# Performance work log

Measured on AMD Instinct MI355X. Metric: run time of the kernel, lower is better.

## Reference

```python
import jax, jax.numpy as jnp
import numpy as np

N_HEAD = 16
D_MODEL = 1024
B, C = 4, 2048

def setup_inputs() -> dict:
    key = jax.random.key(0)
    k_x, k_wq, k_bq, k_wo, k_bo = jax.random.split(key, 5)
    s = 0.02
    return {
        "x": jax.random.normal(k_x, (B, C, D_MODEL), dtype=jnp.float32),
        "W_qkv": jax.random.normal(k_wq, (D_MODEL, 3 * D_MODEL), dtype=jnp.float32) * s,
        "b_qkv": jax.random.normal(k_bq, (3 * D_MODEL,), dtype=jnp.float32) * s,
        "W_o": jax.random.normal(k_wo, (D_MODEL, D_MODEL), dtype=jnp.float32) * s,
        "b_o": jax.random.normal(k_bo, (D_MODEL,), dtype=jnp.float32) * s,
    }

def reference(x, W_qkv, b_qkv, W_o, b_o):
    Bsz, Cq, D = x.shape
    H = N_HEAD
    hd = D // H
    qkv = x @ W_qkv + b_qkv                      # [B,C,3D]
    Q, K, V = jnp.split(qkv, 3, axis=2)
    # [B,C,H,hd] -> [B,H,C,hd]
    Q = Q.reshape(Bsz, Cq, H, hd).transpose(0, 2, 1, 3)
    K = K.reshape(Bsz, Cq, H, hd).transpose(0, 2, 1, 3)
    V = V.reshape(Bsz, Cq, H, hd).transpose(0, 2, 1, 3)
    scale = 1.0 / np.sqrt(hd).astype(np.float32)
    att = jnp.einsum('bhqd,bhkd->bhqk', Q, K) * scale
    causal = jnp.tril(jnp.ones((Cq, Cq), dtype=bool))
    att = jnp.where(causal, att, jnp.float32(-jnp.inf))
    att = jax.nn.softmax(att, axis=-1)           # dropout = identity (eval)
    out = jnp.einsum('bhqk,bhkd->bhqd', att, V)  # [B,H,C,hd]
    out = out.transpose(0, 2, 1, 3).reshape(Bsz, Cq, D)
    return out @ W_o + b_o
```

## Files before the change

### kernel.cpp

```cpp
#include <hip/hip_runtime.h>
#include <hip/hip_bf16.h>

typedef __attribute__((ext_vector_type(8))) short bf16x8;
typedef __attribute__((ext_vector_type(4))) float f32x4;

#define NH 16
#define DM 1024
#define HD 64
#define CSEQ 2048
#define MROWS 8192
#define NBH 64

static __device__ __forceinline__ unsigned short f2bf(float f) {
  __hip_bfloat16 h = __float2bfloat16(f);
  return *reinterpret_cast<unsigned short*>(&h);
}

static __device__ __forceinline__ short bf_qscale(short s) {
  unsigned u = ((unsigned)(unsigned short)s) << 16;
  float f = __builtin_bit_cast(float, u) * 0.18033688f;
  return (short)f2bf(f);
}

static __device__ __forceinline__ void gload_lds16(const void* g, void* l) {
  __builtin_amdgcn_global_load_lds(
      (const __attribute__((address_space(1))) unsigned int*)g,
      (__attribute__((address_space(3))) unsigned int*)l, 16, 0, 0);
}

__global__ __launch_bounds__(256) void cast_f32_bf16(const float* __restrict__ in,
                                                     unsigned short* __restrict__ out,
                                                     int n4) {
  int stride = gridDim.x * blockDim.x;
  for (int i = blockIdx.x * blockDim.x + threadIdx.x; i < n4; i += stride) {
    float4 v = ((const float4*)in)[i];
    ushort4 o;
    o.x = f2bf(v.x); o.y = f2bf(v.y); o.z = f2bf(v.z); o.w = f2bf(v.w);
    ((ushort4*)out)[i] = o;
  }
}

__global__ __launch_bounds__(256) void transpose_cast(const float* __restrict__ src,
                                                      unsigned short* __restrict__ dst,
                                                      int K, int N) {
  __shared__ float tile[32][33];
  int tx = threadIdx.x, ty = threadIdx.y;
  int n0 = blockIdx.x * 32, k0 = blockIdx.y * 32;
  #pragma unroll
  for (int i = 0; i < 32; i += 8)
    tile[ty + i][tx] = src[(size_t)(k0 + ty + i) * N + n0 + tx];
  __syncthreads();
  #pragma unroll
  for (int i = 0; i < 32; i += 8)
    dst[(size_t)(n0 + ty + i) * K + k0 + tx] = f2bf(tile[tx][ty + i]);
}

template<int CNT>
static __device__ __forceinline__ void ld_frags(const char* base, int r0, int cx, int g,
                                                bf16x8 (*out)[2]) {
  #pragma unroll
  for (int i = 0; i < CNT; i++) {
    int row = r0 + i * 16 + cx;
    #pragma unroll
    for (int kc = 0; kc < 2; kc++)
      out[i][kc] = *(const bf16x8*)(base + row * 128 + ((((kc << 2) | g) ^ (row & 7)) << 4));
  }
}

#define BARR() __builtin_amdgcn_s_barrier()
#define LGKM0() asm volatile("s_waitcnt lgkmcnt(0)" ::: "memory")
#define VMCNT8() asm volatile("s_waitcnt vmcnt(8)" ::: "memory")
#define VMCNT0() asm volatile("s_waitcnt vmcnt(0)" ::: "memory")
#define PRIO1() __builtin_amdgcn_s_setprio(1)
#define PRIO0() __builtin_amdgcn_s_setprio(0)

static __device__ __forceinline__ void mfma_pair(const bf16x8 af[4][2], const bf16x8 bf2[2][2],
                                                 f32x4 acc[4][4], int n0) {
  #pragma unroll
  for (int kc = 0; kc < 2; kc++)
    #pragma unroll
    for (int mi = 0; mi < 4; mi++)
      #pragma unroll
      for (int ni = 0; ni < 2; ni++)
        acc[mi][n0 + ni] = __builtin_amdgcn_mfma_f32_16x16x32_bf16(
            af[mi][kc], bf2[ni][kc], acc[mi][n0 + ni], 0, 0, 0);
}

template<int MODE>
__global__ __launch_bounds__(256, 2) void gemm128d(const unsigned short* __restrict__ A,
                                                   const unsigned short* __restrict__ BT,
                                                   const float* __restrict__ bias,
                                                   float* __restrict__ outF,
                                                   unsigned short* __restrict__ outQKV,
                                                   int N, int K) {
  __shared__ char sA[2][16384];
  __shared__ char sB[2][16384];
  int tid = threadIdx.x;
  int w = tid >> 6, l = tid & 63, g = l >> 4, cx = l & 15;
  int wm = (w >> 1) * 64, wn = (w & 1) * 64;

  int nwgx = gridDim.x;
  int nwg = nwgx * gridDim.y;
  int gid = blockIdx.y * nwgx + blockIdx.x;
  int swz = (gid & 7) * (nwg >> 3) + (gid >> 3);
  int bm = (swz / nwgx) * 128, bn = (swz % nwgx) * 128;

  const unsigned short* Ap[4];
  const unsigned short* Bp[4];
  #pragma unroll
  for (int i = 0; i < 4; i++) {
    int c = tid + i * 256;
    int ar = c >> 3, as = ((c & 7) ^ (ar & 7)) * 8;
    Ap[i] = A + (size_t)(bm + ar) * K + as;
    Bp[i] = BT + (size_t)(bn + ar) * K + as;
  }

  #define STAGE_AB(t, buf) do { int ko_ = (t) << 6;                 \
      gload_lds16(Ap[0] + ko_, sA[buf] + (tid)       * 16);         \
      gload_lds16(Ap[1] + ko_, sA[buf] + (tid + 256) * 16);         \
      gload_lds16(Ap[2] + ko_, sA[buf] + (tid + 512) * 16);         \
      gload_lds16(Ap[3] + ko_, sA[buf] + (tid + 768) * 16);         \
      gload_lds16(Bp[0] + ko_, sB[buf] + (tid)       * 16);         \
      gload_lds16(Bp[1] + ko_, sB[buf] + (tid + 256) * 16);         \
      gload_lds16(Bp[2] + ko_, sB[buf] + (tid + 512) * 16);         \
      gload_lds16(Bp[3] + ko_, sB[buf] + (tid + 768) * 16);         \
    } while (0)

  f32x4 acc[4][4];
  #pragma unroll
  for (int i = 0; i < 4; i++)
    #pragma unroll
    for (int j = 0; j < 4; j++) acc[i][j] = (f32x4){0.f, 0.f, 0.f, 0.f};

  int NT = K >> 6;

  STAGE_AB(0, 0);
  STAGE_AB(1, 1);
  VMCNT8();
  BARR();

  int cur = 0;
  for (int t = 0; t < NT; t++) {
    const char* Ac = sA[cur];
    const char* Bc = sB[cur];
    bool h1 = (t + 1) < NT, h2 = (t + 2) < NT;
    bf16x8 af[4][2], bfr[4][2];

    ld_frags<4>(Ac, wm, cx, g, af);
    ld_frags<4>(Bc, wn, cx, g, bfr);
    BARR(); LGKM0();
    PRIO1(); mfma_pair(af, &bfr[0], acc, 0); PRIO0();
    BARR();

    if (h2) STAGE_AB(t + 2, cur);
    PRIO1(); mfma_pair(af, &bfr[2], acc, 2); PRIO0();
    if (h2)      { VMCNT8(); }
    else if (h1) { VMCNT0(); }
    BARR();
    cur ^= 1;
  }

  #pragma unroll
  for (int mi = 0; mi < 4; mi++) {
    #pragma unroll
    for (int ni = 0; ni < 4; ni++) {
      int col = bn + wn + ni * 16 + cx;
      float bv = bias[col];
      int row0 = bm + wm + mi * 16 + g * 4;
      #pragma unroll
      for (int r = 0; r < 4; r++) {
        float v = acc[mi][ni][r] + bv;
        int rr = row0 + r;
        if (MODE == 0) {
          outF[(size_t)rr * N + col] = v;
        } else {
          int which = col >> 10, rem = col & 1023;
          int h = rem >> 6, d = rem & 63;
          int b = rr >> 11, cq = rr & 2047;
          if (which == 2) {
            int pos = (cq & ~31) + (((cq >> 2) & 3) << 3) + (((cq >> 4) & 1) << 2) + (cq & 3);
            outQKV[((size_t)2 * NBH + b * NH + h) * (CSEQ * HD) +
                   (size_t)d * CSEQ + pos] = f2bf(v);
          } else {
            outQKV[((size_t)which * NBH + b * NH + h) * (CSEQ * HD) + (size_t)cq * HD + d] = f2bf(v);
          }
        }
      }
    }
  }
  #undef STAGE_AB
}

__global__ __launch_bounds__(256, 2) void attn_kernel(const unsigned short* __restrict__ Qb,
                                                      const unsigned short* __restrict__ Kb,
                                                      const unsigned short* __restrict__ VTb,
                                                      unsigned short* __restrict__ O) {
  __shared__ char sKb[2][16384];
  __shared__ char sVt[2][16384];
  int tid = threadIdx.x;
  int w = tid >> 6, l = tid & 63, g = l >> 4, cx = l & 15;
  int gid = blockIdx.x;
  int bh = ((gid >> 7) << 3) | (gid & 7);
  int qt = 15 - ((gid >> 3) & 15);

  const unsigned short* Qp  = Qb  + (size_t)bh * CSEQ * HD;
  const unsigned short* Kp  = Kb  + (size_t)bh * CSEQ * HD;
  const unsigned short* VTp = VTb + (size_t)bh * CSEQ * HD;

  bf16x8 qf[2][2];
  #pragma unroll
  for (int qh = 0; qh < 2; qh++) {
    int qrow = qt * 128 + w * 32 + qh * 16 + cx;
    qf[qh][0] = *(const bf16x8*)(Qp + (size_t)qrow * HD + g * 8);
    qf[qh][1] = *(const bf16x8*)(Qp + (size_t)qrow * HD + 32 + g * 8);
    #pragma unroll
    for (int kc = 0; kc < 2; kc++)
      #pragma unroll
      for (int j = 0; j < 8; j++) qf[qh][kc][j] = bf_qscale(qf[qh][kc][j]);
  }

  f32x4 o[2][4];
  #pragma unroll
  for (int qh = 0; qh < 2; qh++)
    #pragma unroll
    for (int nf2 = 0; nf2 < 4; nf2++) o[qh][nf2] = (f32x4){0.f, 0.f, 0.f, 0.f};
  float mrow[2] = {-INFINITY, -INFINITY}, lrow[2] = {0.f, 0.f};

  const unsigned short* Ksrc[4];
  const unsigned short* Vsrc[4];
  #pragma unroll
  for (int i = 0; i < 4; i++) {
    int c = tid + i * 256;
    int krow = c >> 3, ksl = (c & 7) ^ (krow & 7);
    int vd = c >> 4, vsl = (c & 15) ^ (vd & 7);
    Ksrc[i] = Kp + (size_t)krow * HD + ksl * 8;
    Vsrc[i] = VTp + (size_t)vd * CSEQ + vsl * 8;
  }

  #define ATT_STAGE(koff, voff, buf) do {                              \
      _Pragma("unroll")                                                \
      for (int i_ = 0; i_ < 4; i_++) {                                 \
        gload_lds16(Ksrc[i_] + (koff), sKb[buf] + (tid + i_ * 256) * 16); \
        gload_lds16(Vsrc[i_] + (voff), sVt[buf] + (tid + i_ * 256) * 16); \
      } } while (0)

  ATT_STAGE((size_t)0, (size_t)0, 0);
  __syncthreads();
  int cur = 0;

  for (int kt = 0; kt <= qt; kt++) {
    if (kt < qt) {
      size_t ko = (size_t)(kt + 1) * 128 * HD;
      size_t vo = (size_t)(kt + 1) * 128;
      ATT_STAGE(ko, vo, cur ^ 1);
    }
    const char* Kc = sKb[cur];
    const char* Vc = sVt[cur];

    f32x4 sacc[2][8];
    #pragma unroll
    for (int qh = 0; qh < 2; qh++)
      #pragma unroll
      for (int nf = 0; nf < 8; nf++) sacc[qh][nf] = (f32x4){0.f, 0.f, 0.f, 0.f};
    PRIO1();
    #pragma unroll
    for (int kc = 0; kc < 2; kc++) {
      #pragma unroll
      for (int nf = 0; nf < 8; nf++) {
        int row = nf * 16 + cx;
        bf16x8 kf = *(const bf16x8*)(Kc + row * 128 + ((((kc << 2) | g) ^ (row & 7)) << 4));
        sacc[0][nf] = __builtin_amdgcn_mfma_f32_16x16x32_bf16(kf, qf[0][kc], sacc[0][nf], 0, 0, 0);
        sacc[1][nf] = __builtin_amdgcn_mfma_f32_16x16x32_bf16(kf, qf[1][kc], sacc[1][nf], 0, 0, 0);
      }
    }
    PRIO0();

    if (kt == qt) {
      #pragma unroll
      for (int qh = 0; qh < 2; qh++)
        #pragma unroll
        for (int nf = 0; nf < 8; nf++)
          #pragma unroll
          for (int r = 0; r < 4; r++)
            if (nf * 16 + 4 * g + r > w * 32 + qh * 16 + cx) sacc[qh][nf][r] = -INFINITY;
    }
    float mx[2];
    #pragma unroll
    for (int qh = 0; qh < 2; qh++) {
      float m8[8];
      #pragma unroll
      for (int nf = 0; nf < 8; nf++)
        m8[nf] = fmaxf(fmaxf(sacc[qh][nf][0], sacc[qh][nf][1]), fmaxf(sacc[qh][nf][2], sacc[qh][nf][3]));
      float m = fmaxf(fmaxf(fmaxf(m8[0], m8[1]), fmaxf(m8[2], m8[3])),
                      fmaxf(fmaxf(m8[4], m8[5]), fmaxf(m8[6], m8[7])));
      m = fmaxf(m, __shfl_xor(m, 16));
      m = fmaxf(m, __shfl_xor(m, 32));
      mx[qh] = m;
    }

    float need = fmaxf(mx[0] - mrow[0], mx[1] - mrow[1]);
    if (!__all(need <= 8.f)) {
      #pragma unroll
      for (int qh = 0; qh < 2; qh++) {
        float mnew = fmaxf(mrow[qh], mx[qh]);
        float alpha = __builtin_amdgcn_exp2f(mrow[qh] - mnew);
        mrow[qh] = mnew;
        lrow[qh] *= alpha;
        #pragma unroll
        for (int r = 0; r < 4; r++) {
          float ar = __shfl(alpha, (l & 48) | ((l >> 2) & 12) | r);
          #pragma unroll
          for (int nf2 = 0; nf2 < 4; nf2++) o[qh][nf2][r] *= ar;
        }
      }
    }
    #pragma unroll
    for (int qh = 0; qh < 2; qh++) {
      #pragma unroll
      for (int nf = 0; nf < 8; nf++)
        #pragma unroll
        for (int r = 0; r < 4; r++)
          sacc[qh][nf][r] = __builtin_amdgcn_exp2f(sacc[qh][nf][r] - mrow[qh]);
      float s8[8];
      #pragma unroll
      for (int nf = 0; nf < 8; nf++)
        s8[nf] = (sacc[qh][nf][0] + sacc[qh][nf][1]) + (sacc[qh][nf][2] + sacc[qh][nf][3]);
      float sum = ((s8[0] + s8[1]) + (s8[2] + s8[3])) + ((s8[4] + s8[5]) + (s8[6] + s8[7]));
      sum += __shfl_xor(sum, 16);
      sum += __shfl_xor(sum, 32);
      lrow[qh] += sum;
    }

    bf16x8 pa[2][4];
    #pragma unroll
    for (int qh = 0; qh < 2; qh++)
      #pragma unroll
      for (int kc = 0; kc < 4; kc++) {
        #pragma unroll
        for (int j = 0; j < 4; j++) {
          pa[qh][kc][j]     = (short)f2bf(sacc[qh][2 * kc][j]);
          pa[qh][kc][j + 4] = (short)f2bf(sacc[qh][2 * kc + 1][j]);
        }
      }

    PRIO1();
    #pragma unroll
    for (int kc = 0; kc < 4; kc++) {
      #pragma unroll
      for (int nf2 = 0; nf2 < 4; nf2++) {
        int d = nf2 * 16 + cx;
        bf16x8 vf = *(const bf16x8*)(Vc + ((d * 256 + (((kc << 2) | g) << 4)) ^ ((d & 7) << 4)));
        o[0][nf2] = __builtin_amdgcn_mfma_f32_16x16x32_bf16(pa[0][kc], vf, o[0][nf2], 0, 0, 0);
        o[1][nf2] = __builtin_amdgcn_mfma_f32_16x16x32_bf16(pa[1][kc], vf, o[1][nf2], 0, 0, 0);
      }
    }
    PRIO0();

    if (kt < qt) {
      __syncthreads();
      cur ^= 1;
    }
  }

  int b = bh >> 4, hh = bh & 15;
  #pragma unroll
  for (int qh = 0; qh < 2; qh++) {
    float linv = 1.0f / lrow[qh];
    #pragma unroll
    for (int r = 0; r < 4; r++) {
      float inv = __shfl(linv, (l & 48) | ((l >> 2) & 12) | r);
      int q = qt * 128 + w * 32 + qh * 16 + 4 * g + r;
      size_t base = ((size_t)(b * CSEQ + q)) * DM + hh * HD;
      #pragma unroll
      for (int nf2 = 0; nf2 < 4; nf2++)
        O[base + nf2 * 16 + cx] = f2bf(o[qh][nf2][r] * inv);
    }
  }
  #undef ATT_STAGE
}

extern "C" void kernel_launch(void* const* d_in, const int* in_sizes, int n_in,
                              void* d_out, int out_size, void* d_ws, size_t ws_size,
                              hipStream_t stream) {
  const float* x    = (const float*)d_in[0];
  const float* Wqkv = (const float*)d_in[1];
  const float* bqkv = (const float*)d_in[2];
  const float* Wo   = (const float*)d_in[3];
  const float* bo   = (const float*)d_in[4];
  float* out = (float*)d_out;

  unsigned short* ws = (unsigned short*)d_ws;
  const size_t XB_OFF    = 0;
  const size_t WQKVT_OFF = 8388608;
  const size_t WOT_OFF   = WQKVT_OFF + 3145728;
  const size_t QKV_OFF   = WOT_OFF + 1048576;
  const size_t ATT_OFF   = QKV_OFF + 3 * 8388608;

  unsigned short* xb    = ws + XB_OFF;
  unsigned short* wqkvT = ws + WQKVT_OFF;
  unsigned short* woT   = ws + WOT_OFF;
  unsigned short* qkv   = ws + QKV_OFF;
  unsigned short* att   = ws + ATT_OFF;

  cast_f32_bf16<<<2048, 256, 0, stream>>>(x, xb, (MROWS * DM) / 4);
  transpose_cast<<<dim3(3 * DM / 32, DM / 32), dim3(32, 8), 0, stream>>>(Wqkv, wqkvT, DM, 3 * DM);
  transpose_cast<<<dim3(DM / 32, DM / 32), dim3(32, 8), 0, stream>>>(Wo, woT, DM, DM);

  gemm128d<1><<<dim3(3 * DM / 128, MROWS / 128), 256, 0, stream>>>(
      xb, wqkvT, bqkv, nullptr, qkv, 3 * DM, DM);

  attn_kernel<<<dim3(1024), 256, 0, stream>>>(
      qkv, qkv + 8388608, qkv + 16777216, att);

  gemm128d<0><<<dim3(DM / 128, MROWS / 128), 256, 0, stream>>>(
      att, woT, bo, out, nullptr, DM, DM);
}
```

Measured before the change: 205.9 us.

## Use 256-row query tiles with 8 waves and MFMA-based softmax row sums

The attention kernel now uses 512-thread blocks covering 256 query rows, so each K/V tile staged in LDS is shared by twice as many query rows and half as many blocks are launched. The grid mapping is remapped so that pairs of heavy and light causal tiles are interleaved. The softmax denominator is no longer computed with explicit adds and cross-lane shuffles; it is accumulated by an extra MFMA against a vector of ones. This trades more MFMA work and a longer masked tail (two diagonal tiles) for fewer reductions and less K/V global traffic, with occupancy possibly limited by the new launch bounds and register pressure.

```diff
diff --git a/kernel.cpp b/kernel.cpp
--- a/kernel.cpp
+++ b/kernel.cpp
@@ -191,7 +191,7 @@
   #undef STAGE_AB
 }
 
-__global__ __launch_bounds__(256, 2) void attn_kernel(const unsigned short* __restrict__ Qb,
+__global__ __launch_bounds__(512, 4) void attn_kernel(const unsigned short* __restrict__ Qb,
                                                       const unsigned short* __restrict__ Kb,
                                                       const unsigned short* __restrict__ VTb,
                                                       unsigned short* __restrict__ O) {
@@ -200,8 +200,10 @@
   int tid = threadIdx.x;
   int w = tid >> 6, l = tid & 63, g = l >> 4, cx = l & 15;
   int gid = blockIdx.x;
-  int bh = ((gid >> 7) << 3) | (gid & 7);
-  int qt = 15 - ((gid >> 3) & 15);
+  int bh = ((gid >> 6) << 3) | (gid & 7);
+  int qs = (gid >> 3) & 7;
+  int qb = (gid & 256) ? qs : (7 - qs);
+  int NKV = 2 * qb + 2;
 
   const unsigned short* Qp  = Qb  + (size_t)bh * CSEQ * HD;
   const unsigned short* Kp  = Kb  + (size_t)bh * CSEQ * HD;
@@ -210,7 +212,7 @@
   bf16x8 qf[2][2];
   #pragma unroll
   for (int qh = 0; qh < 2; qh++) {
-    int qrow = qt * 128 + w * 32 + qh * 16 + cx;
+    int qrow = qb * 256 + w * 32 + qh * 16 + cx;
     qf[qh][0] = *(const bf16x8*)(Qp + (size_t)qrow * HD + g * 8);
     qf[qh][1] = *(const bf16x8*)(Qp + (size_t)qrow * HD + 32 + g * 8);
     #pragma unroll
@@ -219,40 +221,44 @@
       for (int j = 0; j < 8; j++) qf[qh][kc][j] = bf_qscale(qf[qh][kc][j]);
   }
 
-  f32x4 o[2][4];
-  #pragma unroll
-  for (int qh = 0; qh < 2; qh++)
+  bf16x8 vones;
+  #pragma unroll
+  for (int j = 0; j < 8; j++) vones[j] = (short)0x3F80;
+
+  f32x4 o[2][4], osum[2];
+  #pragma unroll
+  for (int qh = 0; qh < 2; qh++) {
     #pragma unroll
     for (int nf2 = 0; nf2 < 4; nf2++) o[qh][nf2] = (f32x4){0.f, 0.f, 0.f, 0.f};
-  float mrow[2] = {-INFINITY, -INFINITY}, lrow[2] = {0.f, 0.f};
-
-  const unsigned short* Ksrc[4];
-  const unsigned short* Vsrc[4];
-  #pragma unroll
-  for (int i = 0; i < 4; i++) {
-    int c = tid + i * 256;
-    int krow = c >> 3, ksl = (c & 7) ^ (krow & 7);
-    int vd = c >> 4, vsl = (c & 15) ^ (vd & 7);
-    Ksrc[i] = Kp + (size_t)krow * HD + ksl * 8;
-    Vsrc[i] = VTp + (size_t)vd * CSEQ + vsl * 8;
-  }
-
-  #define ATT_STAGE(koff, voff, buf) do {                              \
-      _Pragma("unroll")                                                \
-      for (int i_ = 0; i_ < 4; i_++) {                                 \
-        gload_lds16(Ksrc[i_] + (koff), sKb[buf] + (tid + i_ * 256) * 16); \
-        gload_lds16(Vsrc[i_] + (voff), sVt[buf] + (tid + i_ * 256) * 16); \
-      } } while (0)
-
-  ATT_STAGE((size_t)0, (size_t)0, 0);
+    osum[qh] = (f32x4){0.f, 0.f, 0.f, 0.f};
+  }
+  float mrow[2] = {-INFINITY, -INFINITY};
+
+  int c0 = tid, c1 = tid + 512;
+  int krow0 = c0 >> 3, ksl0 = (c0 & 7) ^ (krow0 & 7);
+  int krow1 = c1 >> 3, ksl1 = (c1 & 7) ^ (krow1 & 7);
+  int vd0 = c0 >> 4, vsl0 = (c0 & 15) ^ (vd0 & 7);
+  int vd1 = c1 >> 4, vsl1 = (c1 & 15) ^ (vd1 & 7);
+  const unsigned short* Ksrc0 = Kp + (size_t)krow0 * HD + ksl0 * 8;
+  const unsigned short* Ksrc1 = Kp + (size_t)krow1 * HD + ksl1 * 8;
+  const unsigned short* Vsrc0 = VTp + (size_t)vd0 * CSEQ + vsl0 * 8;
+  const unsigned short* Vsrc1 = VTp + (size_t)vd1 * CSEQ + vsl1 * 8;
+
+  gload_lds16(Ksrc0, sKb[0] + c0 * 16);
+  gload_lds16(Ksrc1, sKb[0] + c1 * 16);
+  gload_lds16(Vsrc0, sVt[0] + c0 * 16);
+  gload_lds16(Vsrc1, sVt[0] + c1 * 16);
   __syncthreads();
   int cur = 0;
 
-  for (int kt = 0; kt <= qt; kt++) {
-    if (kt < qt) {
+  for (int kt = 0; kt < NKV; kt++) {
+    if (kt + 1 < NKV) {
       size_t ko = (size_t)(kt + 1) * 128 * HD;
       size_t vo = (size_t)(kt + 1) * 128;
-      ATT_STAGE(ko, vo, cur ^ 1);
+      gload_lds16(Ksrc0 + ko, sKb[cur ^ 1] + c0 * 16);
+      gload_lds16(Ksrc1 + ko, sKb[cur ^ 1] + c1 * 16);
+      gload_lds16(Vsrc0 + vo, sVt[cur ^ 1] + c0 * 16);
+      gload_lds16(Vsrc1 + vo, sVt[cur ^ 1] + c1 * 16);
     }
     const char* Kc = sKb[cur];
     const char* Vc = sVt[cur];
@@ -275,14 +281,16 @@
     }
     PRIO0();
 
-    if (kt == qt) {
-      #pragma unroll
-      for (int qh = 0; qh < 2; qh++)
+    if (kt >= NKV - 2) {
+      #pragma unroll
+      for (int qh = 0; qh < 2; qh++) {
+        int qglob = qb * 256 + w * 32 + qh * 16 + cx;
         #pragma unroll
         for (int nf = 0; nf < 8; nf++)
           #pragma unroll
           for (int r = 0; r < 4; r++)
-            if (nf * 16 + 4 * g + r > w * 32 + qh * 16 + cx) sacc[qh][nf][r] = -INFINITY;
+            if (kt * 128 + nf * 16 + 4 * g + r > qglob) sacc[qh][nf][r] = -INFINITY;
+      }
     }
     float mx[2];
     #pragma unroll
@@ -305,31 +313,22 @@
         float mnew = fmaxf(mrow[qh], mx[qh]);
         float alpha = __builtin_amdgcn_exp2f(mrow[qh] - mnew);
         mrow[qh] = mnew;
-        lrow[qh] *= alpha;
         #pragma unroll
         for (int r = 0; r < 4; r++) {
           float ar = __shfl(alpha, (l & 48) | ((l >> 2) & 12) | r);
           #pragma unroll
           for (int nf2 = 0; nf2 < 4; nf2++) o[qh][nf2][r] *= ar;
+          osum[qh][r] *= ar;
         }
       }
     }
     #pragma unroll
-    for (int qh = 0; qh < 2; qh++) {
+    for (int qh = 0; qh < 2; qh++)
       #pragma unroll
       for (int nf = 0; nf < 8; nf++)
         #pragma unroll
         for (int r = 0; r < 4; r++)
           sacc[qh][nf][r] = __builtin_amdgcn_exp2f(sacc[qh][nf][r] - mrow[qh]);
-      float s8[8];
-      #pragma unroll
-      for (int nf = 0; nf < 8; nf++)
-        s8[nf] = (sacc[qh][nf][0] + sacc[qh][nf][1]) + (sacc[qh][nf][2] + sacc[qh][nf][3]);
-      float sum = ((s8[0] + s8[1]) + (s8[2] + s8[3])) + ((s8[4] + s8[5]) + (s8[6] + s8[7]));
-      sum += __shfl_xor(sum, 16);
-      sum += __shfl_xor(sum, 32);
-      lrow[qh] += sum;
-    }
 
     bf16x8 pa[2][4];
     #pragma unroll
@@ -353,10 +352,12 @@
         o[0][nf2] = __builtin_amdgcn_mfma_f32_16x16x32_bf16(pa[0][kc], vf, o[0][nf2], 0, 0, 0);
         o[1][nf2] = __builtin_amdgcn_mfma_f32_16x16x32_bf16(pa[1][kc], vf, o[1][nf2], 0, 0, 0);
       }
+      osum[0] = __builtin_amdgcn_mfma_f32_16x16x32_bf16(pa[0][kc], vones, osum[0], 0, 0, 0);
+      osum[1] = __builtin_amdgcn_mfma_f32_16x16x32_bf16(pa[1][kc], vones, osum[1], 0, 0, 0);
     }
     PRIO0();
 
-    if (kt < qt) {
+    if (kt + 1 < NKV) {
       __syncthreads();
       cur ^= 1;
     }
@@ -365,18 +366,16 @@
   int b = bh >> 4, hh = bh & 15;
   #pragma unroll
   for (int qh = 0; qh < 2; qh++) {
-    float linv = 1.0f / lrow[qh];
     #pragma unroll
     for (int r = 0; r < 4; r++) {
-      float inv = __shfl(linv, (l & 48) | ((l >> 2) & 12) | r);
-      int q = qt * 128 + w * 32 + qh * 16 + 4 * g + r;
+      float inv = 1.0f / osum[qh][r];
+      int q = qb * 256 + w * 32 + qh * 16 + 4 * g + r;
       size_t base = ((size_t)(b * CSEQ + q)) * DM + hh * HD;
       #pragma unroll
       for (int nf2 = 0; nf2 < 4; nf2++)
         O[base + nf2 * 16 + cx] = f2bf(o[qh][nf2][r] * inv);
     }
   }
-  #undef ATT_STAGE
 }
 
 extern "C" void kernel_launch(void* const* d_in, const int* in_sizes, int n_in,
@@ -409,7 +408,7 @@
   gemm128d<1><<<dim3(3 * DM / 128, MROWS / 128), 256, 0, stream>>>(
       xb, wqkvT, bqkv, nullptr, qkv, 3 * DM, DM);
 
-  attn_kernel<<<dim3(1024), 256, 0, stream>>>(
+  attn_kernel<<<dim3(512), 512, 0, stream>>>(
       qkv, qkv + 8388608, qkv + 16777216, att);
 
   gemm128d<0><<<dim3(DM / 128, MROWS / 128), 256, 0, stream>>>(
```

Result: slower. 305.6 us (+48.4%).
